# Kernel tuning notes

Measured on AMD Instinct MI355X. Metric: run time of the kernel, lower is better.

## Reference

```python
import jax, jax.numpy as jnp
import numpy as np


def _he_scale(k, shape, fan_in):
    return jax.random.normal(k, shape, dtype=jnp.float32) * np.sqrt(2.0 / fan_in).astype(np.float32)


def setup_inputs() -> dict:
    key = jax.random.key(0)
    kx, kt, kp, kg, kf = jax.random.split(key, 5)
    B, H, W, C, D = 4, 64, 64, 256, 128
    x = jax.random.normal(kx, (B, H, W, C), dtype=jnp.float32)
    Wt = _he_scale(kt, (C, D), C)
    Wp = _he_scale(kp, (C, D), C)
    Wg = _he_scale(kg, (C, D), C)
    Wf = _he_scale(kf, (D, C), D)
    return {"x": x, "Wt": Wt, "Wp": Wp, "Wg": Wg, "Wf": Wf}


def _maxpool1d(z, pool_size=2, stride=1):
    # Keras MaxPool1D, padding='valid': output length = (N - pool_size)//stride + 1
    return jax.lax.reduce_window(
        z, -jnp.inf, jax.lax.max,
        window_dimensions=(1, pool_size, 1),
        window_strides=(1, stride, 1),
        padding='VALID')


def reference(x, Wt, Wp, Wg, Wf):
    B, H, W, C = x.shape
    D = Wt.shape[1]
    N = H * W
    # 1x1 conv projections == per-position matmuls
    theta = jnp.einsum('bhwc,cd->bhwd', x, Wt).reshape(B, N, D)   # [B,N,D]
    phi = jnp.einsum('bhwc,cd->bhwd', x, Wp).reshape(B, N, D)     # [B,N,D]
    g = jnp.einsum('bhwc,cd->bhwd', x, Wg).reshape(B, N, D)       # [B,N,D]
    # embedded mode: subsample phi and g (pool_size=2, strides=1) -> M = N-1
    phi = _maxpool1d(phi)                                          # [B,M,D]
    g = _maxpool1d(g)                                              # [B,M,D]
    # f = theta @ phi^T, softmax over keys (no scaling in embedded mode)
    f = jax.nn.softmax(jnp.einsum('bnd,bmd->bnm', theta, phi), axis=-1)  # [B,N,M]
    y = jnp.einsum('bnm,bmd->bnd', f, g).reshape(B, H, W, D)       # [B,H,W,D]
    # final 1x1 conv back to C channels + residual
    z = x + jnp.einsum('bhwd,dc->bhwc', y, Wf)
    return z
```

## Files before the change

### kernel.cpp

```cpp
#include <hip/hip_runtime.h>

#define B_  4
#define N_  4096
#define C_  256
#define D_  128
#define M_  4095
#define BN_ (B_ * N_)

typedef _Float16 half_t;
typedef __attribute__((ext_vector_type(8))) _Float16 half8;
typedef __attribute__((ext_vector_type(4))) _Float16 half4;
typedef __attribute__((ext_vector_type(4))) float f32x4;

#define MFMA16x16x32(A, B, C) __builtin_amdgcn_mfma_f32_16x16x32_f16(A, B, C, 0, 0, 0)
#define LOG2E 1.44269504088896f
#define RTHR  5.0f

__global__ __launch_bounds__(256) void prep_kernel(
    const float* __restrict__ Wt, const float* __restrict__ Wp,
    const float* __restrict__ Wg, const float* __restrict__ Wf,
    half_t* __restrict__ WT_hi, half_t* __restrict__ WfT)
{
    const int idx = blockIdx.x * 256 + threadIdx.x;
    const int wsel = blockIdx.y;
    if (wsel < 3) {
        const float* __restrict__ W = (wsel == 0) ? Wt : (wsel == 1) ? Wp : Wg;
        const int d = idx >> 8, c = idx & 255;
        WT_hi[(size_t)wsel * 32768 + idx] = (half_t)W[(size_t)c * D_ + d];
    } else {
        const int c = idx >> 7, d = idx & 127;
        WfT[idx] = (half_t)Wf[(size_t)d * C_ + c];
    }
}

__global__ __launch_bounds__(256) void proj_kernel(
    const float* __restrict__ x, const half_t* __restrict__ WT_hi,
    half_t* __restrict__ theta, half_t* __restrict__ pphi,
    half_t* __restrict__ pgT)
{
    const int tid = threadIdx.x;
    const int lane = tid & 63;
    const int w = tid >> 6;
    const int lm = lane & 15;
    const int lq = lane >> 4;
    const int r0 = blockIdx.x * 64;
    const int which = blockIdx.y;
    const half_t* __restrict__ Wg_ = WT_hi + (size_t)which * 32768;

    __shared__ __align__(16) unsigned char lds_raw[18432];
    half_t (*Xh)[40]  = (half_t (*)[40])(lds_raw);
    half_t (*Whl)[40] = (half_t (*)[40])(lds_raw + 5120);

    f32x4 acc[8];
#pragma unroll
    for (int nb = 0; nb < 8; ++nb)
#pragma unroll
        for (int r = 0; r < 4; ++r) acc[nb][r] = 0.f;

    const int xr = tid >> 2, xc = (tid & 3) * 8;
    const int wr = tid >> 1, wc = (tid & 1) * 16;

    const float* xs = x + (size_t)(r0 + xr) * C_ + xc;
    const half_t* wsrc = Wg_ + (size_t)wr * 256 + wc;
    float4 xv0 = *(const float4*)&xs[0];
    float4 xv1 = *(const float4*)&xs[4];
    half8 wv0 = *(const half8*)&wsrc[0];
    half8 wv1 = *(const half8*)&wsrc[8];

    for (int kc = 0; kc < 8; ++kc) {
        half8 hi;
        hi[0] = (half_t)xv0.x; hi[1] = (half_t)xv0.y;
        hi[2] = (half_t)xv0.z; hi[3] = (half_t)xv0.w;
        hi[4] = (half_t)xv1.x; hi[5] = (half_t)xv1.y;
        hi[6] = (half_t)xv1.z; hi[7] = (half_t)xv1.w;
        half8 w0 = wv0, w1 = wv1;
        __syncthreads();
        *(half8*)&Xh[xr][xc] = hi;
        *(half8*)&Whl[wr][wc]     = w0;
        *(half8*)&Whl[wr][wc + 8] = w1;
        if (kc < 7) {
            xs += 32; wsrc += 32;
            xv0 = *(const float4*)&xs[0];
            xv1 = *(const float4*)&xs[4];
            wv0 = *(const half8*)&wsrc[0];
            wv1 = *(const half8*)&wsrc[8];
        }
        __syncthreads();

        half8 ah = *(const half8*)&Xh[w * 16 + lm][lq * 8];
#pragma unroll
        for (int nb = 0; nb < 8; ++nb) {
            half8 bh = *(const half8*)&Whl[nb * 16 + lm][lq * 8];
            acc[nb] = MFMA16x16x32(ah, bh, acc[nb]);
        }
    }

    if (which == 0) {
#pragma unroll
        for (int nb = 0; nb < 8; ++nb)
#pragma unroll
            for (int r = 0; r < 4; ++r)
                theta[(size_t)(r0 + w * 16 + lq * 4 + r) * D_ + nb * 16 + lm] =
                    (half_t)(acc[nb][r] * LOG2E);
        return;
    }

    __syncthreads();
    half_t (*LsT)[72] = (half_t (*)[72])(lds_raw);
#pragma unroll
    for (int nb = 0; nb < 8; ++nb) {
        const int d = nb * 16 + lm;
        const int m = w * 16 + lq * 4;
        half4 pk;
#pragma unroll
        for (int r = 0; r < 4; ++r) pk[r] = (half_t)acc[nb][r];
        *(half4*)&LsT[d][m] = pk;
    }
    if (tid < 128) {
        int rh = r0 + 64;
        if ((rh & (N_ - 1)) == 0) rh = r0 + 63;
        const float* xrow = x + (size_t)rh * C_;
        const half_t* wrow = Wg_ + (size_t)tid * 256;
        float s = 0.f;
#pragma unroll
        for (int c8 = 0; c8 < 32; ++c8) {
            half8 h = *(const half8*)&wrow[c8 * 8];
            float4 xa = *(const float4*)&xrow[c8 * 8];
            float4 xb = *(const float4*)&xrow[c8 * 8 + 4];
            s += xa.x * (float)h[0] + xa.y * (float)h[1]
               + xa.z * (float)h[2] + xa.w * (float)h[3]
               + xb.x * (float)h[4] + xb.y * (float)h[5]
               + xb.z * (float)h[6] + xb.w * (float)h[7];
        }
        LsT[tid][64] = (half_t)s;
    }
    __syncthreads();

    if (which == 1) {
        const int m = tid >> 2, dh = (tid & 3) * 32;
        half8 o[4];
#pragma unroll
        for (int j = 0; j < 32; ++j) {
            float v0 = (float)LsT[dh + j][m];
            float v1 = (float)LsT[dh + j][m + 1];
            o[j >> 3][j & 7] = (half_t)fmaxf(v0, v1);
        }
        half8* dst = (half8*)&pphi[(size_t)(r0 + m) * D_ + dh];
#pragma unroll
        for (int j = 0; j < 4; ++j) dst[j] = o[j];
    } else {
        const int d = tid >> 1, mh = (tid & 1) * 32;
        const int b = r0 / N_, m0 = r0 & (N_ - 1);
        half8 in[4];
#pragma unroll
        for (int j = 0; j < 4; ++j) in[j] = *(const half8*)&LsT[d][mh + j * 8];
        const half_t ext = LsT[d][mh + 32];
        half8 o[4];
#pragma unroll
        for (int j = 0; j < 32; ++j) {
            float v0 = (float)in[j >> 3][j & 7];
            float v1 = (j == 31) ? (float)ext : (float)in[(j + 1) >> 3][(j + 1) & 7];
            o[j >> 3][j & 7] = (half_t)fmaxf(v0, v1);
        }
        half8* dst = (half8*)&pgT[((size_t)b * D_ + d) * N_ + m0 + mh];
#pragma unroll
        for (int j = 0; j < 4; ++j) dst[j] = o[j];
    }
}

template<int KS>
__global__ __launch_bounds__(256, 2) void attn_kernel(
    const half_t* __restrict__ theta, const half_t* __restrict__ pphi,
    const half_t* __restrict__ pgT, half_t* __restrict__ ypart,
    float* __restrict__ mstat, float* __restrict__ lstat)
{
    const int TILES = 64 / KS;
    const int tid = threadIdx.x;
    const int lane = tid & 63;
    const int w = tid >> 6;
    const int lm = lane & 15;
    const int lq = lane >> 4;
    const int qt = blockIdx.x, ksb = blockIdx.y, b = blockIdx.z;
    const int q0 = qt * 128;
    const int kt0 = ksb * TILES, kt1 = kt0 + TILES;

    __shared__ half_t Ks[64][136];
    __shared__ half_t Gts[128][72];
    __shared__ half_t Ps[128][72];

    half8 qh[2][4];
#pragma unroll
    for (int nb = 0; nb < 2; ++nb) {
        const half_t* tr_ = theta + ((size_t)b * N_ + q0 + w * 32 + nb * 16 + lm) * D_;
#pragma unroll
        for (int k4 = 0; k4 < 4; ++k4)
            qh[nb][k4] = *(const half8*)(tr_ + k4 * 32 + lq * 8);
    }

    const int key = tid >> 2, ch = tid & 3;
    const int gdd = tid >> 1, gkh = tid & 1;
    const float4* ksrc = (const float4*)(pphi +
        ((size_t)b * N_ + kt0 * 64 + key) * D_ + ch * 32);
    const float4* gsrc = (const float4*)(pgT +
        ((size_t)b * D_ + gdd) * N_ + kt0 * 64 + gkh * 32);

    float m_i[2] = {-1e30f, -1e30f};
    float l_i[2] = {0.f, 0.f};
    f32x4 yacc[2][8];
#pragma unroll
    for (int mb = 0; mb < 2; ++mb)
#pragma unroll
        for (int dn = 0; dn < 8; ++dn)
#pragma unroll
            for (int r = 0; r < 4; ++r) yacc[mb][dn][r] = 0.f;

    for (int kt = kt0; kt < kt1; ++kt) {
        const int k0 = kt * 64;
        __syncthreads();
        {
            float4 a0 = ksrc[0], a1 = ksrc[1], a2 = ksrc[2], a3 = ksrc[3];
            float4 g0 = gsrc[0], g1 = gsrc[1], g2 = gsrc[2], g3 = gsrc[3];
            ksrc += 1024;
            gsrc += 8;
            float4* kdst = (float4*)&Ks[key][ch * 32];
            kdst[0] = a0; kdst[1] = a1; kdst[2] = a2; kdst[3] = a3;
            float4* gdst = (float4*)&Gts[gdd][gkh * 32];
            gdst[0] = g0; gdst[1] = g1; gdst[2] = g2; gdst[3] = g3;
        }
        __syncthreads();

        f32x4 sc[4][2];
#pragma unroll
        for (int kb = 0; kb < 4; ++kb)
#pragma unroll
            for (int nb = 0; nb < 2; ++nb)
#pragma unroll
                for (int r = 0; r < 4; ++r) sc[kb][nb][r] = 0.f;
        __builtin_amdgcn_s_setprio(1);
#pragma unroll
        for (int kb = 0; kb < 4; ++kb) {
#pragma unroll
            for (int k4 = 0; k4 < 4; ++k4) {
                half8 kf = *(const half8*)&Ks[kb * 16 + lm][k4 * 32 + lq * 8];
#pragma unroll
                for (int nb = 0; nb < 2; ++nb)
                    sc[kb][nb] = MFMA16x16x32(kf, qh[nb][k4], sc[kb][nb]);
            }
        }
        __builtin_amdgcn_s_setprio(0);
        if (k0 + 64 > M_) {
#pragma unroll
            for (int kb = 0; kb < 4; ++kb)
#pragma unroll
                for (int r = 0; r < 4; ++r)
                    if (k0 + kb * 16 + lq * 4 + r >= M_) {
                        sc[kb][0][r] = -1e30f; sc[kb][1][r] = -1e30f;
                    }
        }

        float mt[2];
#pragma unroll
        for (int nb = 0; nb < 2; ++nb) {
            float m0 = -1e30f;
#pragma unroll
            for (int kb = 0; kb < 4; ++kb)
#pragma unroll
                for (int r = 0; r < 4; ++r) m0 = fmaxf(m0, sc[kb][nb][r]);
            m0 = fmaxf(m0, __shfl_xor(m0, 16, 64));
            m0 = fmaxf(m0, __shfl_xor(m0, 32, 64));
            mt[nb] = m0;
        }
        const bool need0 = __any(mt[0] > m_i[0] + RTHR);
        const bool need1 = __any(mt[1] > m_i[1] + RTHR);
        float alphav[2] = {1.f, 1.f};
#pragma unroll
        for (int nb = 0; nb < 2; ++nb) {
            const bool need = nb ? need1 : need0;
            float mnew = m_i[nb];
            if (need) {
                mnew = fmaxf(m_i[nb], mt[nb]);
                alphav[nb] = exp2f(m_i[nb] - mnew);
                m_i[nb] = mnew;
            }
            float rs = 0.f;
#pragma unroll
            for (int kb = 0; kb < 4; ++kb) {
                half4 pk;
#pragma unroll
                for (int r = 0; r < 4; ++r) {
                    float p = exp2f(sc[kb][nb][r] - mnew);
                    rs += p;
                    pk[r] = (half_t)p;
                }
                *(half4*)&Ps[w * 32 + nb * 16 + lm][kb * 16 + lq * 4] = pk;
            }
            l_i[nb] = l_i[nb] * alphav[nb] + rs;
        }
        if (need0) {
            float a_t[4];
#pragma unroll
            for (int r = 0; r < 4; ++r) a_t[r] = __shfl(alphav[0], lq * 4 + r, 16);
#pragma unroll
            for (int dn = 0; dn < 8; ++dn)
#pragma unroll
                for (int r = 0; r < 4; ++r) yacc[0][dn][r] *= a_t[r];
        }
        if (need1) {
            float a_t[4];
#pragma unroll
            for (int r = 0; r < 4; ++r) a_t[r] = __shfl(alphav[1], lq * 4 + r, 16);
#pragma unroll
            for (int dn = 0; dn < 8; ++dn)
#pragma unroll
                for (int r = 0; r < 4; ++r) yacc[1][dn][r] *= a_t[r];
        }

        half8 pf[2][2];
#pragma unroll
        for (int mb = 0; mb < 2; ++mb)
#pragma unroll
            for (int k2 = 0; k2 < 2; ++k2)
                pf[mb][k2] = *(const half8*)&Ps[w * 32 + mb * 16 + lm][k2 * 32 + lq * 8];
        __builtin_amdgcn_s_setprio(1);
#pragma unroll
        for (int dn = 0; dn < 8; ++dn) {
#pragma unroll
            for (int k2 = 0; k2 < 2; ++k2) {
                half8 gf = *(const half8*)&Gts[dn * 16 + lm][k2 * 32 + lq * 8];
                yacc[0][dn] = MFMA16x16x32(pf[0][k2], gf, yacc[0][dn]);
                yacc[1][dn] = MFMA16x16x32(pf[1][k2], gf, yacc[1][dn]);
            }
        }
        __builtin_amdgcn_s_setprio(0);
    }

#pragma unroll
    for (int nb = 0; nb < 2; ++nb) {
        l_i[nb] += __shfl_xor(l_i[nb], 16, 64);
        l_i[nb] += __shfl_xor(l_i[nb], 32, 64);
    }
    half_t* yp = ypart + ((size_t)ksb * BN_ + (size_t)b * N_) * D_;
#pragma unroll
    for (int mb = 0; mb < 2; ++mb)
#pragma unroll
        for (int dn = 0; dn < 8; ++dn)
#pragma unroll
            for (int r = 0; r < 4; ++r)
                yp[(size_t)(q0 + w * 32 + mb * 16 + lq * 4 + r) * D_ + dn * 16 + lm] =
                    (half_t)yacc[mb][dn][r];
    if (lq == 0) {
#pragma unroll
        for (int nb = 0; nb < 2; ++nb) {
            const int row = q0 + w * 32 + nb * 16 + lm;
            mstat[(size_t)ksb * BN_ + (size_t)b * N_ + row] = m_i[nb];
            lstat[(size_t)ksb * BN_ + (size_t)b * N_ + row] = l_i[nb];
        }
    }
}

template<int KS>
__global__ __launch_bounds__(256) void final_kernel(
    const half_t* __restrict__ ypart, const float* __restrict__ mstat,
    const float* __restrict__ lstat, const float* __restrict__ x,
    const half_t* __restrict__ WfT, float* __restrict__ out)
{
    const int tid = threadIdx.x;
    const int lane = tid & 63;
    const int w = tid >> 6;
    const int lm = lane & 15;
    const int lq = lane >> 4;
    const int r0 = blockIdx.x * 64;
    const int c0 = blockIdx.y * 64;

    __shared__ half_t Ys[64][136];
    __shared__ half_t Wfs[64][136];
    __shared__ float scl[KS][64];

    if (tid < 64) {
        const int row = r0 + tid;
        float mv[KS], lv[KS], wv[KS];
        float Mx = -1e30f;
#pragma unroll
        for (int s = 0; s < KS; ++s) {
            mv[s] = mstat[(size_t)s * BN_ + row];
            lv[s] = lstat[(size_t)s * BN_ + row];
            Mx = fmaxf(Mx, mv[s]);
        }
        float lsum = 0.f;
#pragma unroll
        for (int s = 0; s < KS; ++s) { wv[s] = exp2f(mv[s] - Mx); lsum += wv[s] * lv[s]; }
        const float inv = 1.f / lsum;
#pragma unroll
        for (int s = 0; s < KS; ++s) scl[s][tid] = wv[s] * inv;
    }
    __syncthreads();

    {
        const int sr = tid >> 2;
        const int dd = (tid & 3) * 32;
        float ss[KS];
#pragma unroll
        for (int s = 0; s < KS; ++s) ss[s] = scl[s][sr];
        const size_t yb = (size_t)(r0 + sr) * D_ + dd;
        half8 o[4];
#pragma unroll
        for (int q = 0; q < 4; ++q) {
            float m[8];
#pragma unroll
            for (int j = 0; j < 8; ++j) m[j] = 0.f;
#pragma unroll
            for (int s = 0; s < KS; ++s) {
                half8 yv = *(const half8*)&ypart[(size_t)s * BN_ * D_ + yb + q * 8];
#pragma unroll
                for (int j = 0; j < 8; ++j) m[j] += ss[s] * (float)yv[j];
            }
#pragma unroll
            for (int j = 0; j < 8; ++j) o[q][j] = (half_t)m[j];
        }
#pragma unroll
        for (int q = 0; q < 4; ++q) *(half8*)&Ys[sr][dd + q * 8] = o[q];
        const half_t* wf = WfT + (size_t)(c0 + sr) * D_ + dd;
#pragma unroll
        for (int q = 0; q < 4; ++q)
            *(half8*)&Wfs[sr][dd + q * 8] = *(const half8*)&wf[q * 8];
    }
    __syncthreads();

    f32x4 acc[4];
#pragma unroll
    for (int nb = 0; nb < 4; ++nb)
#pragma unroll
        for (int r = 0; r < 4; ++r) acc[nb][r] = 0.f;

#pragma unroll
    for (int k4 = 0; k4 < 4; ++k4) {
        half8 af = *(const half8*)&Ys[w * 16 + lm][k4 * 32 + lq * 8];
#pragma unroll
        for (int nb = 0; nb < 4; ++nb) {
            half8 bf = *(const half8*)&Wfs[nb * 16 + lm][k4 * 32 + lq * 8];
            acc[nb] = MFMA16x16x32(af, bf, acc[nb]);
        }
    }

#pragma unroll
    for (int nb = 0; nb < 4; ++nb)
#pragma unroll
        for (int r = 0; r < 4; ++r) {
            const int row = r0 + w * 16 + lq * 4 + r;
            const int col = c0 + nb * 16 + lm;
            out[(size_t)row * C_ + col] =
                acc[nb][r] + x[(size_t)row * C_ + col];
        }
}

extern "C" void kernel_launch(void* const* d_in, const int* in_sizes, int n_in,
                              void* d_out, int out_size, void* d_ws, size_t ws_size,
                              hipStream_t stream)
{
    const float* x  = (const float*)d_in[0];
    const float* Wt = (const float*)d_in[1];
    const float* Wp = (const float*)d_in[2];
    const float* Wg = (const float*)d_in[3];
    const float* Wf = (const float*)d_in[4];
    float* out = (float*)d_out;

    const size_t SEG = (size_t)BN_ * D_;

    const size_t need8 = (3 + 8) * SEG * 2 + (size_t)2 * 8 * BN_ * 4 + 131072 * 2;
    const int KS = (ws_size >= need8) ? 8 : 4;

    half_t* hb    = (half_t*)d_ws;
    half_t* theta = hb;
    half_t* pphi  = hb + SEG;
    half_t* pgT   = hb + 2 * SEG;
    half_t* ypart = hb + 3 * SEG;
    float*  mstat = (float*)(hb + (size_t)(3 + KS) * SEG);
    float*  lstat = mstat + (size_t)KS * BN_;
    half_t* WT_hi = (half_t*)(lstat + (size_t)KS * BN_);
    half_t* WfT   = WT_hi + 3 * 32768;

    prep_kernel<<<dim3(128, 4), 256, 0, stream>>>(Wt, Wp, Wg, Wf, WT_hi, WfT);
    proj_kernel<<<dim3(BN_ / 64, 3), 256, 0, stream>>>(x, WT_hi, theta, pphi, pgT);
    if (KS == 8) {
        attn_kernel<8><<<dim3(N_ / 128, 8, B_), 256, 0, stream>>>(
            theta, pphi, pgT, ypart, mstat, lstat);
        final_kernel<8><<<dim3(BN_ / 64, 4), 256, 0, stream>>>(
            ypart, mstat, lstat, x, WfT, out);
    } else {
        attn_kernel<4><<<dim3(N_ / 128, 4, B_), 256, 0, stream>>>(
            theta, pphi, pgT, ypart, mstat, lstat);
        final_kernel<4><<<dim3(BN_ / 64, 4), 256, 0, stream>>>(
            ypart, mstat, lstat, x, WfT, out);
    }
}
```

Baseline: 178.6 us.

## Swizzle LDS tiles in attention and final kernels, widen final column tile

```diff
diff --git a/kernel.cpp b/kernel.cpp
--- a/kernel.cpp
+++ b/kernel.cpp
@@ -15,6 +15,8 @@
 #define MFMA16x16x32(A, B, C) __builtin_amdgcn_mfma_f32_16x16x32_f16(A, B, C, 0, 0, 0)
 #define LOG2E 1.44269504088896f
 #define RTHR  5.0f
+
+#define SWZ(r, c) ((c) ^ (((r) & 7) << 3))
 
 __global__ __launch_bounds__(256) void prep_kernel(
     const float* __restrict__ Wt, const float* __restrict__ Wp,
@@ -169,7 +171,7 @@
 }
 
 template<int KS>
-__global__ __launch_bounds__(256, 2) void attn_kernel(
+__global__ __launch_bounds__(256, 3) void attn_kernel(
     const half_t* __restrict__ theta, const half_t* __restrict__ pphi,
     const half_t* __restrict__ pgT, half_t* __restrict__ ypart,
     float* __restrict__ mstat, float* __restrict__ lstat)
@@ -184,9 +186,9 @@
     const int q0 = qt * 128;
     const int kt0 = ksb * TILES, kt1 = kt0 + TILES;
 
-    __shared__ half_t Ks[64][136];
-    __shared__ half_t Gts[128][72];
-    __shared__ half_t Ps[128][72];
+    __shared__ half_t Ks[64][128];
+    __shared__ half_t Gts[128][64];
+    __shared__ half_t Ps[128][64];
 
     half8 qh[2][4];
 #pragma unroll
@@ -222,10 +224,14 @@
             float4 g0 = gsrc[0], g1 = gsrc[1], g2 = gsrc[2], g3 = gsrc[3];
             ksrc += 1024;
             gsrc += 8;
-            float4* kdst = (float4*)&Ks[key][ch * 32];
-            kdst[0] = a0; kdst[1] = a1; kdst[2] = a2; kdst[3] = a3;
-            float4* gdst = (float4*)&Gts[gdd][gkh * 32];
-            gdst[0] = g0; gdst[1] = g1; gdst[2] = g2; gdst[3] = g3;
+            *(float4*)&Ks[key][SWZ(key, ch * 32 +  0)] = a0;
+            *(float4*)&Ks[key][SWZ(key, ch * 32 +  8)] = a1;
+            *(float4*)&Ks[key][SWZ(key, ch * 32 + 16)] = a2;
+            *(float4*)&Ks[key][SWZ(key, ch * 32 + 24)] = a3;
+            *(float4*)&Gts[gdd][SWZ(gdd, gkh * 32 +  0)] = g0;
+            *(float4*)&Gts[gdd][SWZ(gdd, gkh * 32 +  8)] = g1;
+            *(float4*)&Gts[gdd][SWZ(gdd, gkh * 32 + 16)] = g2;
+            *(float4*)&Gts[gdd][SWZ(gdd, gkh * 32 + 24)] = g3;
         }
         __syncthreads();
 
@@ -239,9 +245,10 @@
         __builtin_amdgcn_s_setprio(1);
 #pragma unroll
         for (int kb = 0; kb < 4; ++kb) {
+            const int krow = kb * 16 + lm;
 #pragma unroll
             for (int k4 = 0; k4 < 4; ++k4) {
-                half8 kf = *(const half8*)&Ks[kb * 16 + lm][k4 * 32 + lq * 8];
+                half8 kf = *(const half8*)&Ks[krow][SWZ(krow, k4 * 32 + lq * 8)];
 #pragma unroll
                 for (int nb = 0; nb < 2; ++nb)
                     sc[kb][nb] = MFMA16x16x32(kf, qh[nb][k4], sc[kb][nb]);
@@ -283,6 +290,7 @@
                 m_i[nb] = mnew;
             }
             float rs = 0.f;
+            const int prow = w * 32 + nb * 16 + lm;
 #pragma unroll
             for (int kb = 0; kb < 4; ++kb) {
                 half4 pk;
@@ -292,7 +300,7 @@
                     rs += p;
                     pk[r] = (half_t)p;
                 }
-                *(half4*)&Ps[w * 32 + nb * 16 + lm][kb * 16 + lq * 4] = pk;
+                *(half4*)&Ps[prow][SWZ(prow, kb * 16 + lq * 4)] = pk;
             }
             l_i[nb] = l_i[nb] * alphav[nb] + rs;
         }
@@ -317,16 +325,19 @@
 
         half8 pf[2][2];
 #pragma unroll
-        for (int mb = 0; mb < 2; ++mb)
+        for (int mb = 0; mb < 2; ++mb) {
+            const int prow = w * 32 + mb * 16 + lm;
 #pragma unroll
             for (int k2 = 0; k2 < 2; ++k2)
-                pf[mb][k2] = *(const half8*)&Ps[w * 32 + mb * 16 + lm][k2 * 32 + lq * 8];
+                pf[mb][k2] = *(const half8*)&Ps[prow][SWZ(prow, k2 * 32 + lq * 8)];
+        }
         __builtin_amdgcn_s_setprio(1);
 #pragma unroll
         for (int dn = 0; dn < 8; ++dn) {
+            const int grow = dn * 16 + lm;
 #pragma unroll
             for (int k2 = 0; k2 < 2; ++k2) {
-                half8 gf = *(const half8*)&Gts[dn * 16 + lm][k2 * 32 + lq * 8];
+                half8 gf = *(const half8*)&Gts[grow][SWZ(grow, k2 * 32 + lq * 8)];
                 yacc[0][dn] = MFMA16x16x32(pf[0][k2], gf, yacc[0][dn]);
                 yacc[1][dn] = MFMA16x16x32(pf[1][k2], gf, yacc[1][dn]);
             }
@@ -370,10 +381,10 @@
     const int lm = lane & 15;
     const int lq = lane >> 4;
     const int r0 = blockIdx.x * 64;
-    const int c0 = blockIdx.y * 64;
-
-    __shared__ half_t Ys[64][136];
-    __shared__ half_t Wfs[64][136];
+    const int c0 = blockIdx.y * 128;
+
+    __shared__ half_t Ys[64][128];
+    __shared__ half_t Wfs[128][128];
     __shared__ float scl[KS][64];
 
     if (tid < 64) {
@@ -393,6 +404,13 @@
 #pragma unroll
         for (int s = 0; s < KS; ++s) scl[s][tid] = wv[s] * inv;
     }
+    {
+        const int wc = tid >> 1, wd = (tid & 1) * 64;
+        const half_t* wf = WfT + (size_t)(c0 + wc) * D_ + wd;
+#pragma unroll
+        for (int q = 0; q < 8; ++q)
+            *(half8*)&Wfs[wc][SWZ(wc, wd + q * 8)] = *(const half8*)&wf[q * 8];
+    }
     __syncthreads();
 
     {
@@ -418,32 +436,30 @@
             for (int j = 0; j < 8; ++j) o[q][j] = (half_t)m[j];
         }
 #pragma unroll
-        for (int q = 0; q < 4; ++q) *(half8*)&Ys[sr][dd + q * 8] = o[q];
-        const half_t* wf = WfT + (size_t)(c0 + sr) * D_ + dd;
-#pragma unroll
-        for (int q = 0; q < 4; ++q)
-            *(half8*)&Wfs[sr][dd + q * 8] = *(const half8*)&wf[q * 8];
+        for (int q = 0; q < 4; ++q) *(half8*)&Ys[sr][SWZ(sr, dd + q * 8)] = o[q];
     }
     __syncthreads();
 
-    f32x4 acc[4];
-#pragma unroll
-    for (int nb = 0; nb < 4; ++nb)
+    f32x4 acc[8];
+#pragma unroll
+    for (int nb = 0; nb < 8; ++nb)
 #pragma unroll
         for (int r = 0; r < 4; ++r) acc[nb][r] = 0.f;
 
+    const int yrow = w * 16 + lm;
 #pragma unroll
     for (int k4 = 0; k4 < 4; ++k4) {
-        half8 af = *(const half8*)&Ys[w * 16 + lm][k4 * 32 + lq * 8];
-#pragma unroll
-        for (int nb = 0; nb < 4; ++nb) {
-            half8 bf = *(const half8*)&Wfs[nb * 16 + lm][k4 * 32 + lq * 8];
+        half8 af = *(const half8*)&Ys[yrow][SWZ(yrow, k4 * 32 + lq * 8)];
+#pragma unroll
+        for (int nb = 0; nb < 8; ++nb) {
+            const int wrow = nb * 16 + lm;
+            half8 bf = *(const half8*)&Wfs[wrow][SWZ(wrow, k4 * 32 + lq * 8)];
             acc[nb] = MFMA16x16x32(af, bf, acc[nb]);
         }
     }
 
 #pragma unroll
-    for (int nb = 0; nb < 4; ++nb)
+    for (int nb = 0; nb < 8; ++nb)
 #pragma unroll
         for (int r = 0; r < 4; ++r) {
             const int row = r0 + w * 16 + lq * 4 + r;
@@ -484,12 +500,12 @@
     if (KS == 8) {
         attn_kernel<8><<<dim3(N_ / 128, 8, B_), 256, 0, stream>>>(
             theta, pphi, pgT, ypart, mstat, lstat);
-        final_kernel<8><<<dim3(BN_ / 64, 4), 256, 0, stream>>>(
+        final_kernel<8><<<dim3(BN_ / 64, 2), 256, 0, stream>>>(
             ypart, mstat, lstat, x, WfT, out);
     } else {
         attn_kernel<4><<<dim3(N_ / 128, 4, B_), 256, 0, stream>>>(
             theta, pphi, pgT, ypart, mstat, lstat);
-        final_kernel<4><<<dim3(BN_ / 64, 4), 256, 0, stream>>>(
+        final_kernel<4><<<dim3(BN_ / 64, 2), 256, 0, stream>>>(
             ypart, mstat, lstat, x, WfT, out);
     }
 }
```

After: 174.4 us. 1.02x faster.

## Split split-K merge into separate kernel and widen final GEMM tile with swizzled LDS

Applied to the files above, without the earlier changes.

```diff
diff --git a/kernel.cpp b/kernel.cpp
--- a/kernel.cpp
+++ b/kernel.cpp
@@ -15,6 +15,8 @@
 #define MFMA16x16x32(A, B, C) __builtin_amdgcn_mfma_f32_16x16x32_f16(A, B, C, 0, 0, 0)
 #define LOG2E 1.44269504088896f
 #define RTHR  5.0f
+
+#define SWZ(r, c) ((c) ^ (((r) & 7) << 3))
 
 __global__ __launch_bounds__(256) void prep_kernel(
     const float* __restrict__ Wt, const float* __restrict__ Wp,
@@ -359,9 +361,50 @@
 }
 
 template<int KS>
+__global__ __launch_bounds__(256) void merge_kernel(
+    const half_t* __restrict__ ypart, const float* __restrict__ mstat,
+    const float* __restrict__ lstat, half_t* __restrict__ ymerged)
+{
+    const int idx = blockIdx.x * 256 + threadIdx.x;
+    const int row = idx >> 2;
+    const int dd = (idx & 3) * 32;
+
+    float mv[KS], lv[KS], wv[KS];
+    float Mx = -1e30f;
+#pragma unroll
+    for (int s = 0; s < KS; ++s) {
+        mv[s] = mstat[(size_t)s * BN_ + row];
+        lv[s] = lstat[(size_t)s * BN_ + row];
+        Mx = fmaxf(Mx, mv[s]);
+    }
+    float lsum = 0.f;
+#pragma unroll
+    for (int s = 0; s < KS; ++s) { wv[s] = exp2f(mv[s] - Mx); lsum += wv[s] * lv[s]; }
+    const float inv = 1.f / lsum;
+#pragma unroll
+    for (int s = 0; s < KS; ++s) wv[s] *= inv;
+
+    const size_t yb = (size_t)row * D_ + dd;
+#pragma unroll
+    for (int q = 0; q < 4; ++q) {
+        float m[8];
+#pragma unroll
+        for (int j = 0; j < 8; ++j) m[j] = 0.f;
+#pragma unroll
+        for (int s = 0; s < KS; ++s) {
+            half8 yv = *(const half8*)&ypart[(size_t)s * BN_ * D_ + yb + q * 8];
+#pragma unroll
+            for (int j = 0; j < 8; ++j) m[j] += wv[s] * (float)yv[j];
+        }
+        half8 o;
+#pragma unroll
+        for (int j = 0; j < 8; ++j) o[j] = (half_t)m[j];
+        *(half8*)&ymerged[yb + q * 8] = o;
+    }
+}
+
 __global__ __launch_bounds__(256) void final_kernel(
-    const half_t* __restrict__ ypart, const float* __restrict__ mstat,
-    const float* __restrict__ lstat, const float* __restrict__ x,
+    const half_t* __restrict__ ymerged, const float* __restrict__ x,
     const half_t* __restrict__ WfT, float* __restrict__ out)
 {
     const int tid = threadIdx.x;
@@ -370,80 +413,48 @@
     const int lm = lane & 15;
     const int lq = lane >> 4;
     const int r0 = blockIdx.x * 64;
-    const int c0 = blockIdx.y * 64;
-
-    __shared__ half_t Ys[64][136];
-    __shared__ half_t Wfs[64][136];
-    __shared__ float scl[KS][64];
-
-    if (tid < 64) {
-        const int row = r0 + tid;
-        float mv[KS], lv[KS], wv[KS];
-        float Mx = -1e30f;
-#pragma unroll
-        for (int s = 0; s < KS; ++s) {
-            mv[s] = mstat[(size_t)s * BN_ + row];
-            lv[s] = lstat[(size_t)s * BN_ + row];
-            Mx = fmaxf(Mx, mv[s]);
-        }
-        float lsum = 0.f;
-#pragma unroll
-        for (int s = 0; s < KS; ++s) { wv[s] = exp2f(mv[s] - Mx); lsum += wv[s] * lv[s]; }
-        const float inv = 1.f / lsum;
-#pragma unroll
-        for (int s = 0; s < KS; ++s) scl[s][tid] = wv[s] * inv;
-    }
-    __syncthreads();
-
+    const int c0 = blockIdx.y * 128;
+
+    __shared__ half_t Ys[64][128];
+    __shared__ half_t Wfs[128][128];
+
+    {
+        const int wc = tid >> 1, wd = (tid & 1) * 64;
+        const half_t* wf = WfT + (size_t)(c0 + wc) * D_ + wd;
+#pragma unroll
+        for (int q = 0; q < 8; ++q)
+            *(half8*)&Wfs[wc][SWZ(wc, wd + q * 8)] = *(const half8*)&wf[q * 8];
+    }
     {
         const int sr = tid >> 2;
         const int dd = (tid & 3) * 32;
-        float ss[KS];
-#pragma unroll
-        for (int s = 0; s < KS; ++s) ss[s] = scl[s][sr];
-        const size_t yb = (size_t)(r0 + sr) * D_ + dd;
-        half8 o[4];
-#pragma unroll
-        for (int q = 0; q < 4; ++q) {
-            float m[8];
-#pragma unroll
-            for (int j = 0; j < 8; ++j) m[j] = 0.f;
-#pragma unroll
-            for (int s = 0; s < KS; ++s) {
-                half8 yv = *(const half8*)&ypart[(size_t)s * BN_ * D_ + yb + q * 8];
-#pragma unroll
-                for (int j = 0; j < 8; ++j) m[j] += ss[s] * (float)yv[j];
-            }
-#pragma unroll
-            for (int j = 0; j < 8; ++j) o[q][j] = (half_t)m[j];
-        }
-#pragma unroll
-        for (int q = 0; q < 4; ++q) *(half8*)&Ys[sr][dd + q * 8] = o[q];
-        const half_t* wf = WfT + (size_t)(c0 + sr) * D_ + dd;
+        const half_t* ym = ymerged + (size_t)(r0 + sr) * D_ + dd;
 #pragma unroll
         for (int q = 0; q < 4; ++q)
-            *(half8*)&Wfs[sr][dd + q * 8] = *(const half8*)&wf[q * 8];
+            *(half8*)&Ys[sr][SWZ(sr, dd + q * 8)] = *(const half8*)&ym[q * 8];
     }
     __syncthreads();
 
-    f32x4 acc[4];
-#pragma unroll
-    for (int nb = 0; nb < 4; ++nb)
+    f32x4 acc[8];
+#pragma unroll
+    for (int nb = 0; nb < 8; ++nb)
 #pragma unroll
         for (int r = 0; r < 4; ++r) acc[nb][r] = 0.f;
 
+    const int yrow = w * 16 + lm;
 #pragma unroll
     for (int k4 = 0; k4 < 4; ++k4) {
-        half8 af = *(const half8*)&Ys[w * 16 + lm][k4 * 32 + lq * 8];
-#pragma unroll
-        for (int nb = 0; nb < 4; ++nb) {
-            half8 bf = *(const half8*)&Wfs[nb * 16 + lm][k4 * 32 + lq * 8];
+        half8 af = *(const half8*)&Ys[yrow][SWZ(yrow, k4 * 32 + lq * 8)];
+#pragma unroll
+        for (int nb = 0; nb < 8; ++nb) {
+            const int wrow = nb * 16 + lm;
+            half8 bf = *(const half8*)&Wfs[wrow][SWZ(wrow, k4 * 32 + lq * 8)];
             acc[nb] = MFMA16x16x32(af, bf, acc[nb]);
         }
     }
 
 #pragma unroll
-    for (int nb = 0; nb < 4; ++nb)
+    for (int nb = 0; nb < 8; ++nb)
 #pragma unroll
         for (int r = 0; r < 4; ++r) {
             const int row = r0 + w * 16 + lq * 4 + r;
@@ -466,30 +477,33 @@
 
     const size_t SEG = (size_t)BN_ * D_;
 
-    const size_t need8 = (3 + 8) * SEG * 2 + (size_t)2 * 8 * BN_ * 4 + 131072 * 2;
+    const size_t need8 = (size_t)(3 + 8 + 1) * SEG * 2
+                       + (size_t)2 * 8 * BN_ * 4 + 131072 * 2;
     const int KS = (ws_size >= need8) ? 8 : 4;
 
-    half_t* hb    = (half_t*)d_ws;
-    half_t* theta = hb;
-    half_t* pphi  = hb + SEG;
-    half_t* pgT   = hb + 2 * SEG;
-    half_t* ypart = hb + 3 * SEG;
-    float*  mstat = (float*)(hb + (size_t)(3 + KS) * SEG);
-    float*  lstat = mstat + (size_t)KS * BN_;
-    half_t* WT_hi = (half_t*)(lstat + (size_t)KS * BN_);
-    half_t* WfT   = WT_hi + 3 * 32768;
+    half_t* hb      = (half_t*)d_ws;
+    half_t* theta   = hb;
+    half_t* pphi    = hb + SEG;
+    half_t* pgT     = hb + 2 * SEG;
+    half_t* ypart   = hb + 3 * SEG;
+    half_t* ymerged = hb + (size_t)(3 + KS) * SEG;
+    float*  mstat   = (float*)(hb + (size_t)(3 + KS + 1) * SEG);
+    float*  lstat   = mstat + (size_t)KS * BN_;
+    half_t* WT_hi   = (half_t*)(lstat + (size_t)KS * BN_);
+    half_t* WfT     = WT_hi + 3 * 32768;
 
     prep_kernel<<<dim3(128, 4), 256, 0, stream>>>(Wt, Wp, Wg, Wf, WT_hi, WfT);
     proj_kernel<<<dim3(BN_ / 64, 3), 256, 0, stream>>>(x, WT_hi, theta, pphi, pgT);
     if (KS == 8) {
         attn_kernel<8><<<dim3(N_ / 128, 8, B_), 256, 0, stream>>>(
             theta, pphi, pgT, ypart, mstat, lstat);
-        final_kernel<8><<<dim3(BN_ / 64, 4), 256, 0, stream>>>(
-            ypart, mstat, lstat, x, WfT, out);
+        merge_kernel<8><<<dim3(BN_ * 4 / 256), 256, 0, stream>>>(
+            ypart, mstat, lstat, ymerged);
     } else {
         attn_kernel<4><<<dim3(N_ / 128, 4, B_), 256, 0, stream>>>(
             theta, pphi, pgT, ypart, mstat, lstat);
-        final_kernel<4><<<dim3(BN_ / 64, 4), 256, 0, stream>>>(
-            ypart, mstat, lstat, x, WfT, out);
-    }
+        merge_kernel<4><<<dim3(BN_ * 4 / 256), 256, 0, stream>>>(
+            ypart, mstat, lstat, ymerged);
+    }
+    final_kernel<<<dim3(BN_ / 64, 2), 256, 0, stream>>>(ymerged, x, WfT, out);
 }
```

New measurement: 175.0 us. 2.1% less time.
